# Performance work log

Hardware: AMD Instinct MI355X
Metric: run time of the kernel (lower is better)

## Reference

```python
import jax, jax.numpy as jnp
import numpy as np

B, T, D, H = 8, 2048, 1024, 128

def setup_inputs() -> dict:
    key = jax.random.key(0)
    ks = jax.random.split(key, 8)
    s = 1.0 / np.sqrt(D)
    return {
        "x": jax.random.normal(ks[0], (B, T, D), dtype=jnp.float32),
        "att": jax.random.normal(ks[1], (B, T, D), dtype=jnp.float32),
        "Wk": jax.random.uniform(ks[2], (D, H), minval=-s, maxval=s, dtype=jnp.float32),
        "bk": jax.random.uniform(ks[3], (H,), minval=-s, maxval=s, dtype=jnp.float32),
        "Wq": jax.random.uniform(ks[4], (D, H), minval=-s, maxval=s, dtype=jnp.float32),
        "bq": jax.random.uniform(ks[5], (H,), minval=-s, maxval=s, dtype=jnp.float32),
        "Wv": jax.random.uniform(ks[6], (D, H), minval=-s, maxval=s, dtype=jnp.float32),
        "bv": jax.random.uniform(ks[7], (H,), minval=-s, maxval=s, dtype=jnp.float32),
    }

def reference(x, att, Wk, bk, Wq, bq, Wv, bv):
    # k, q from `att`; v from `x` (as in the original module)
    k = jnp.einsum('btd,dh->bth', att, Wk) + bk   # [B,T,H]
    q = jnp.einsum('btd,dh->bth', att, Wq) + bq   # [B,T,H]
    v = jnp.einsum('btd,dh->bth', x, Wv) + bv     # [B,T,H]
    # Faithful to source: scores / head_size**(-0.5) == scores * sqrt(head_size)
    scale = jnp.asarray(k.shape[-1], jnp.float32) ** 0.5
    scores = jnp.einsum('bqh,bkh->bqk', q, k) * scale  # [B,T,T]
    att_mat = jax.nn.softmax(scores, axis=-1)
    # dropout p=0.0 -> identity (eval semantics)
    return jnp.einsum('bqk,bkh->bqh', att_mat, v)      # [B,T,H]
```

## Files before the change

kernel.cpp:

```cpp
#include <hip/hip_runtime.h>
#include <stdint.h>

typedef unsigned short u16;
typedef __attribute__((ext_vector_type(8))) short bf16x8;
typedef __attribute__((ext_vector_type(4))) float f32x4;
typedef __attribute__((ext_vector_type(16))) float f32x16;
typedef __attribute__((ext_vector_type(4))) uint32_t u32x4;
typedef __attribute__((ext_vector_type(2))) int int2v;

#define T_LEN 2048
#define D_DIM 1024
#define H_DIM 128
#define SCALE_LOG2 16.32223116f

#define EXP2F(x) __builtin_amdgcn_exp2f(x)

__device__ __forceinline__ u16 f2bf(float f) {
  uint32_t u = __float_as_uint(f);
  u += 0x7FFFu + ((u >> 16) & 1u);
  return (u16)(u >> 16);
}
__device__ __forceinline__ float bf2f(u16 h) { return __uint_as_float(((uint32_t)h) << 16); }

__device__ __forceinline__ void gload16(const void* g, void* l) {
  __builtin_amdgcn_global_load_lds(
      (const __attribute__((address_space(1))) uint32_t*)(uintptr_t)g,
      (__attribute__((address_space(3))) uint32_t*)(uint32_t)(uintptr_t)l,
      16, 0, 0);
}

#define VMCNT0() asm volatile("s_waitcnt vmcnt(0)" ::: "memory")
#define VMLG0() asm volatile("s_waitcnt vmcnt(0) lgkmcnt(0)" ::: "memory")
#define BAR() __builtin_amdgcn_s_barrier()
#define PRIO(n) __builtin_amdgcn_s_setprio(n)

#define MFMA(a, b, c) __builtin_amdgcn_mfma_f32_16x16x32_bf16((a), (b), (c), 0, 0, 0)
#define MFMA32(a, b, c) __builtin_amdgcn_mfma_f32_32x32x16_bf16((a), (b), (c), 0, 0, 0)

__device__ __forceinline__ uint32_t cvtpk(float lo, float hi) {
  uint32_t r;
  asm("v_cvt_pk_bf16_f32 %0, %1, %2" : "=v"(r) : "v"(lo), "v"(hi));
  return r;
}
__device__ __forceinline__ void plswap(uint32_t& a, uint32_t& b, int hi) {
#if __has_builtin(__builtin_amdgcn_permlane32_swap)
  int2v r = __builtin_amdgcn_permlane32_swap((int)a, (int)b, false, false);
  a = (uint32_t)r.x;
  b = (uint32_t)r.y;
#else
  uint32_t as = (uint32_t)__shfl_xor((int)a, 32);
  uint32_t bs = (uint32_t)__shfl_xor((int)b, 32);
  uint32_t na = hi ? bs : a;
  uint32_t nb = hi ? b : as;
  a = na;
  b = nb;
#endif
}

__global__ __launch_bounds__(256) void prep_w(
    const float* __restrict__ Wk, const float* __restrict__ Wq, const float* __restrict__ Wv,
    u16* __restrict__ wqh, u16* __restrict__ wql,
    u16* __restrict__ wkh, u16* __restrict__ wkl,
    u16* __restrict__ wvh) {
  __shared__ u16 th[3][128][16];
  __shared__ u16 tl[2][128][16];
  const int i = threadIdx.x;
  const int d0 = blockIdx.x * 16;
  const int dl = i >> 4;
  const int hb = (i & 15) * 8;
  const int d = d0 + dl;
#pragma unroll
  for (int e = 0; e < 8; ++e) {
    int h = hb + e;
    float q = Wq[d * H_DIM + h] * SCALE_LOG2;
    float k = Wk[d * H_DIM + h];
    float v = Wv[d * H_DIM + h];
    u16 qh = f2bf(q); th[0][h][dl] = qh; tl[0][h][dl] = f2bf(q - bf2f(qh));
    u16 kh = f2bf(k); th[1][h][dl] = kh; tl[1][h][dl] = f2bf(k - bf2f(kh));
    th[2][h][dl] = f2bf(v);
  }
  __syncthreads();
  const int h = i >> 1, c = i & 1;
  u16* planes[5] = {wqh, wql, wkh, wkl, wvh};
  const u16* srcs[5] = {&th[0][0][0], &tl[0][0][0], &th[1][0][0], &tl[1][0][0], &th[2][0][0]};
#pragma unroll
  for (int p = 0; p < 5; ++p) {
    bf16x8 v8 = *(const bf16x8*)(srcs[p] + h * 16 + c * 8);
    *(bf16x8*)(planes[p] + h * 1024 + d0 + c * 8) = v8;
  }
}

#define QBUF 53248

__global__ __launch_bounds__(512) void qkv_proj(
    const float* __restrict__ att, const float* __restrict__ x,
    const u16* __restrict__ wqh, const u16* __restrict__ wql,
    const u16* __restrict__ wkh, const u16* __restrict__ wkl,
    const u16* __restrict__ wvh,
    const float* __restrict__ bq, const float* __restrict__ bk, const float* __restrict__ bv,
    u16* __restrict__ qhp, u16* __restrict__ qlp,
    u16* __restrict__ khp, u16* __restrict__ klp,
    u16* __restrict__ vtp) {
  __shared__ __attribute__((aligned(128))) char lds[104 * 1024];

  const int tid = threadIdx.x;
  const int wid = tid >> 6;
  const int ln = tid & 63;
  const int g = ln >> 4;
  const int cl = ln & 15;
  const int t0g = blockIdx.x * 64;

  const f32x4 fz = {0.f, 0.f, 0.f, 0.f};
  f32x4 accq[4], acck[4], accv[4];
#pragma unroll
  for (int s = 0; s < 4; ++s) { accq[s] = fz; acck[s] = fz; accv[s] = fz; }

  const int isA = tid < 256;
  const int at = tid & 255;
  const int arow = at >> 2;
  const int ac = at & 3;
  const float* srcp = (isA ? att : x) + (size_t)(t0g + arow) * D_DIM + ac * 8;
  const int aw_off = (isA ? 0 : 8192) + arow * 64 + ((ac ^ ((arow >> 1) & 3)) * 16);

  auto STAGE_W = [&](int b, int ks) {
    char* wt = lds + b * QBUF + 12288;
#pragma unroll
    for (int j = 0; j < 5; ++j) {
      int seg = wid * 5 + j;
      int p = seg >> 3;
      int s = seg & 7;
      int db = s * 1024 + ln * 16;
      int row = db >> 6;
      int c = (db >> 4) & 3;
      int cs = c ^ ((row >> 1) & 3);
      const u16* wp = (p == 0) ? wqh : (p == 1) ? wql : (p == 2) ? wkh : (p == 3) ? wkl : wvh;
      gload16(wp + row * 1024 + ks * 32 + cs * 8, wt + p * 8192 + s * 1024);
    }
  };
  auto CWRITE_A = [&](int b, f32x4 f0, f32x4 f1) {
    bf16x8 vh, vl;
#pragma unroll
    for (int e = 0; e < 4; ++e) {
      u16 h0 = f2bf(f0[e]); vh[e] = (short)h0; vl[e] = (short)f2bf(f0[e] - bf2f(h0));
      u16 h1 = f2bf(f1[e]); vh[e + 4] = (short)h1; vl[e + 4] = (short)f2bf(f1[e] - bf2f(h1));
    }
    char* dst = lds + b * QBUF + aw_off;
    *(bf16x8*)dst = vh;
    if (isA) *(bf16x8*)(dst + 4096) = vl;
  };

  {
    f32x4 f0 = *(const f32x4*)(srcp);
    f32x4 f1 = *(const f32x4*)(srcp + 4);
    STAGE_W(0, 0);
    CWRITE_A(0, f0, f1);
  }
  f32x4 pA0 = *(const f32x4*)(srcp + 32);
  f32x4 pA1 = *(const f32x4*)(srcp + 36);
  VMLG0();
  BAR();

  int cur = 0;
  for (int ks = 0; ks < 32; ++ks) {
    f32x4 nA0, nA1;
    if (ks < 30) {
      nA0 = *(const f32x4*)(srcp + (ks + 2) * 32);
      nA1 = *(const f32x4*)(srcp + (ks + 2) * 32 + 4);
    }
    if (ks < 31) STAGE_W(cur ^ 1, ks + 1);
    char* base = lds + cur * QBUF;
    char* wt = base + 12288;
    bf16x8 ah[4], al[4], xh[4];
#pragma unroll
    for (int s = 0; s < 4; ++s) {
      int row = s * 16 + cl;
      int byte = row * 64 + ((g ^ ((row >> 1) & 3)) * 16);
      ah[s] = *(const bf16x8*)(base + byte);
      al[s] = *(const bf16x8*)(base + 4096 + byte);
      xh[s] = *(const bf16x8*)(base + 8192 + byte);
    }
    {
      int hrow = wid * 16 + cl;
      int wb = hrow * 64 + ((g ^ ((hrow >> 1) & 3)) * 16);
      bf16x8 bqh_ = *(const bf16x8*)(wt + 0 * 8192 + wb);
      bf16x8 bql_ = *(const bf16x8*)(wt + 1 * 8192 + wb);
      bf16x8 bkh_ = *(const bf16x8*)(wt + 2 * 8192 + wb);
      bf16x8 bkl_ = *(const bf16x8*)(wt + 3 * 8192 + wb);
      bf16x8 bvh_ = *(const bf16x8*)(wt + 4 * 8192 + wb);
      PRIO(1);
#pragma unroll
      for (int s = 0; s < 4; ++s) {
        accq[s] = MFMA(ah[s], bqh_, accq[s]);
        accq[s] = MFMA(al[s], bqh_, accq[s]);
        accq[s] = MFMA(ah[s], bql_, accq[s]);
        acck[s] = MFMA(ah[s], bkh_, acck[s]);
        acck[s] = MFMA(al[s], bkh_, acck[s]);
        acck[s] = MFMA(ah[s], bkl_, acck[s]);
        accv[s] = MFMA(xh[s], bvh_, accv[s]);
      }
      PRIO(0);
    }
    if (ks < 31) CWRITE_A(cur ^ 1, pA0, pA1);
    pA0 = nA0;
    pA1 = nA1;
    VMLG0();
    BAR();
    cur ^= 1;
  }

  char* vbuf = lds;
  {
    int h = wid * 16 + cl;
    float bqv = bq[h] * SCALE_LOG2, bkv = bk[h], bvv = bv[h];
#pragma unroll
    for (int s = 0; s < 4; ++s) {
#pragma unroll
      for (int r = 0; r < 4; ++r) {
        int t = s * 16 + g * 4 + r;
        size_t idx = (size_t)(t0g + t) * H_DIM + h;
        float qv = accq[s][r] + bqv;
        u16 qh_ = f2bf(qv);
        qhp[idx] = qh_;
        qlp[idx] = f2bf(qv - bf2f(qh_));
        float kv = acck[s][r] + bkv;
        u16 kh_ = f2bf(kv);
        khp[idx] = kh_;
        klp[idx] = f2bf(kv - bf2f(kh_));
        float vv = accv[s][r] + bvv;
        int c3 = t >> 3;
        int byte = h * 128 + ((c3 ^ (h & 7)) * 16) + (t & 7) * 2;
        *(u16*)(vbuf + byte) = f2bf(vv);
      }
    }
  }
  __syncthreads();
  {
    int h = tid >> 2, qtr = tid & 3;
    int b2 = t0g >> 11;
    int tb = t0g & 2047;
    u16* dst = vtp + ((size_t)(b2 * H_DIM + h)) * T_LEN + tb + qtr * 16;
#pragma unroll
    for (int c2 = 0; c2 < 2; ++c2) {
      int c3 = qtr * 2 + c2;
      bf16x8 v8 = *(const bf16x8*)(vbuf + h * 128 + ((c3 ^ (h & 7)) * 16));
      *(bf16x8*)(dst + c2 * 8) = v8;
    }
  }
}

#define KVB 32
#define NT 16

__global__ __launch_bounds__(512, 2) void attn(
    const u16* __restrict__ qhp, const u16* __restrict__ qlp,
    const u16* __restrict__ khp, const u16* __restrict__ klp,
    const u16* __restrict__ vtp,
    float* __restrict__ out) {
  __shared__ __attribute__((aligned(128))) char lds[128 * 1024];

  const int tid = threadIdx.x;
  const int w = tid >> 6;
  const int l = tid & 63;
  const int q5 = l & 31;
  const int hi = l >> 5;
  const int wq = w >> 2;
  const int kvq = w & 3;
  const int pi = wq;
  const int bid = blockIdx.x;
  const int b_ = bid & 7;
  const int t0 = (bid >> 3) * 64;
  const int qrow = t0 + wq * 32 + q5;
  const int kv0q = kvq * 512;

  bf16x8 qh[8], ql[8];
  {
    const u16* qb = qhp + (size_t)(b_ * T_LEN + qrow) * H_DIM + hi * 8;
    const u16* qlb = qlp + (size_t)(b_ * T_LEN + qrow) * H_DIM + hi * 8;
#pragma unroll
    for (int kc = 0; kc < 8; ++kc) {
      qh[kc] = *(const bf16x8*)(qb + kc * 16);
      ql[kc] = *(const bf16x8*)(qlb + kc * 16);
    }
  }

  uint32_t sgoff[8];
#pragma unroll
  for (int i = 0; i < 8; ++i) {
    int gid = i * 128 + pi * 64 + l;
    int plane = gid >> 9;
    int n = gid & 511;
    int row = n >> 4;
    int slot = n & 15;
    int dg = slot ^ (row & 15);
    sgoff[i] = (uint32_t)(plane * 2097152 + (b_ * T_LEN + row) * H_DIM + dg * 8);
  }
  char* const qbuf0 = lds + kvq * 2 * 16384;

  auto STAGE = [&](int b, int kvoff) {
    char* buf = qbuf0 + b * 16384;
#pragma unroll
    for (int i = 0; i < 8; ++i)
      gload16(khp + sgoff[i] + (uint32_t)(kvoff * H_DIM), buf + i * 2048 + pi * 1024);
  };

  f32x16 o[4] = {};
  float m_ = -1e30f;
  float l_ = 0.f;

  STAGE(0, kv0q);
  VMCNT0();
  BAR();

  int cur = 0;
  for (int t = 0; t < NT; ++t) {
    if (t < NT - 1) STAGE(cur ^ 1, kv0q + (t + 1) * KVB);
    bf16x8 vfr[8];
#pragma unroll
    for (int ks = 0; ks < 2; ++ks)
#pragma unroll
      for (int nt = 0; nt < 4; ++nt)
        vfr[ks * 4 + nt] = *(const bf16x8*)(
            vtp + (size_t)(b_ * H_DIM + nt * 32 + q5) * T_LEN +
            kv0q + t * KVB + ks * 16 + hi * 8);

    const char* kb = qbuf0 + cur * 16384 + q5 * 256;
    f32x16 s0 = {}, s1 = {}, s2 = {};
    PRIO(1);
#pragma unroll
    for (int kc = 0; kc < 8; ++kc) {
      int slot = (((kc * 2 + hi) ^ (q5 & 15)) * 16);
      bf16x8 kh_f = *(const bf16x8*)(kb + slot);
      bf16x8 kl_f = *(const bf16x8*)(kb + 8192 + slot);
      s0 = MFMA32(kh_f, qh[kc], s0);
      s1 = MFMA32(kl_f, qh[kc], s1);
      s2 = MFMA32(kh_f, ql[kc], s2);
    }
    PRIO(0);
    f32x16 s = (s0 + s1) + s2;

    float pmax = s[0];
#pragma unroll
    for (int j = 1; j < 16; ++j) pmax = fmaxf(pmax, s[j]);
    pmax = fmaxf(pmax, __shfl_xor(pmax, 32));
    if (__any(pmax > m_ + 8.f)) {
      float mn = fmaxf(m_, pmax);
      float sf = EXP2F(m_ - mn);
      m_ = mn;
      l_ *= sf;
#pragma unroll
      for (int j = 0; j < 16; ++j) {
        int rj = (j & 3) + 8 * (j >> 2) + 4 * hi;
        float sfj = __shfl(sf, rj);
        o[0][j] *= sfj; o[1][j] *= sfj; o[2][j] *= sfj; o[3][j] *= sfj;
      }
    }
    float p[16];
#pragma unroll
    for (int j = 0; j < 16; ++j) p[j] = EXP2F(s[j] - m_);
    float ps = 0.f;
#pragma unroll
    for (int j = 0; j < 16; ++j) ps += p[j];
    ps += __shfl_xor(ps, 32);
    l_ += ps;

    uint32_t u0 = cvtpk(p[0], p[1]), v0 = cvtpk(p[4], p[5]);
    uint32_t u1 = cvtpk(p[2], p[3]), v1 = cvtpk(p[6], p[7]);
    uint32_t u2 = cvtpk(p[8], p[9]), v2 = cvtpk(p[12], p[13]);
    uint32_t u3 = cvtpk(p[10], p[11]), v3 = cvtpk(p[14], p[15]);
    plswap(u0, v0, hi);
    plswap(u1, v1, hi);
    plswap(u2, v2, hi);
    plswap(u3, v3, hi);
    u32x4 f0w = {u0, u1, v0, v1};
    u32x4 f1w = {u2, u3, v2, v3};
    bf16x8 pa0 = *(bf16x8*)&f0w;
    bf16x8 pa1 = *(bf16x8*)&f1w;

    PRIO(1);
#pragma unroll
    for (int nt = 0; nt < 4; ++nt) o[nt] = MFMA32(pa0, vfr[nt], o[nt]);
#pragma unroll
    for (int nt = 0; nt < 4; ++nt) o[nt] = MFMA32(pa1, vfr[4 + nt], o[nt]);
    PRIO(0);

    VMCNT0();
    BAR();
    cur ^= 1;
  }

  float* mlb = (float*)(lds + 96 * 1024);
  __syncthreads();
  if (hi == 0) {
    mlb[(wq * 4 + kvq) * 64 + q5 * 2] = m_;
    mlb[(wq * 4 + kvq) * 64 + q5 * 2 + 1] = l_;
  }
  __syncthreads();
  float sc;
  {
    float ms0 = mlb[(wq * 4 + 0) * 64 + q5 * 2], ls0 = mlb[(wq * 4 + 0) * 64 + q5 * 2 + 1];
    float ms1 = mlb[(wq * 4 + 1) * 64 + q5 * 2], ls1 = mlb[(wq * 4 + 1) * 64 + q5 * 2 + 1];
    float ms2 = mlb[(wq * 4 + 2) * 64 + q5 * 2], ls2 = mlb[(wq * 4 + 2) * 64 + q5 * 2 + 1];
    float ms3 = mlb[(wq * 4 + 3) * 64 + q5 * 2], ls3 = mlb[(wq * 4 + 3) * 64 + q5 * 2 + 1];
    float mM = fmaxf(fmaxf(ms0, ms1), fmaxf(ms2, ms3));
    float L = ls0 * EXP2F(ms0 - mM) + ls1 * EXP2F(ms1 - mM) +
              ls2 * EXP2F(ms2 - mM) + ls3 * EXP2F(ms3 - mM);
    sc = EXP2F(m_ - mM) / L;
  }
#pragma unroll
  for (int j = 0; j < 16; ++j) {
    int rj = (j & 3) + 8 * (j >> 2) + 4 * hi;
    float scj = __shfl(sc, rj);
    o[0][j] *= scj; o[1][j] *= scj; o[2][j] *= scj; o[3][j] *= scj;
  }
  if (kvq != 0) {
    float* ob = (float*)(lds + (wq * 3 + (kvq - 1)) * 16384);
#pragma unroll
    for (int nt = 0; nt < 4; ++nt)
#pragma unroll
      for (int j = 0; j < 16; ++j) ob[nt * 1024 + j * 64 + l] = o[nt][j];
  }
  __syncthreads();
  if (kvq == 0) {
    float* ob0 = (float*)(lds + (wq * 3 + 0) * 16384);
    float* ob1 = (float*)(lds + (wq * 3 + 1) * 16384);
    float* ob2 = (float*)(lds + (wq * 3 + 2) * 16384);
#pragma unroll
    for (int j = 0; j < 16; ++j) {
      int rj = (j & 3) + 8 * (j >> 2) + 4 * hi;
      size_t rbase = (size_t)(b_ * T_LEN + t0 + wq * 32 + rj) * H_DIM + q5;
#pragma unroll
      for (int nt = 0; nt < 4; ++nt) {
        int oi = nt * 1024 + j * 64 + l;
        out[rbase + nt * 32] = o[nt][j] + ob0[oi] + ob1[oi] + ob2[oi];
      }
    }
  }
}

extern "C" void kernel_launch(void* const* d_in, const int* in_sizes, int n_in,
                              void* d_out, int out_size, void* d_ws, size_t ws_size,
                              hipStream_t stream) {
  const float* x   = (const float*)d_in[0];
  const float* att = (const float*)d_in[1];
  const float* Wk  = (const float*)d_in[2];
  const float* bk  = (const float*)d_in[3];
  const float* Wq  = (const float*)d_in[4];
  const float* bq  = (const float*)d_in[5];
  const float* Wv  = (const float*)d_in[6];
  const float* bv  = (const float*)d_in[7];
  float* out = (float*)d_out;
  char* ws = (char*)d_ws;

  u16* wqh = (u16*)(ws);
  u16* wql = (u16*)(ws + 256 * 1024);
  u16* wkh = (u16*)(ws + 512 * 1024);
  u16* wkl = (u16*)(ws + 768 * 1024);
  u16* wvh = (u16*)(ws + 1024 * 1024);
  u16* qhp = (u16*)(ws + (size_t)2 * 1024 * 1024);
  u16* qlp = (u16*)(ws + (size_t)6 * 1024 * 1024);
  u16* khp = (u16*)(ws + (size_t)10 * 1024 * 1024);
  u16* klp = (u16*)(ws + (size_t)14 * 1024 * 1024);
  u16* vtp = (u16*)(ws + (size_t)18 * 1024 * 1024);

  prep_w<<<64, 256, 0, stream>>>(Wk, Wq, Wv, wqh, wql, wkh, wkl, wvh);
  qkv_proj<<<256, 512, 0, stream>>>(att, x, wqh, wql, wkh, wkl, wvh,
                                    bq, bk, bv, qhp, qlp, khp, klp, vtp);
  attn<<<256, 512, 0, stream>>>(qhp, qlp, khp, klp, vtp, out);
}
```

Baseline: 264.0 us.

## Software-pipeline attention so QK of next tile overlaps softmax/PV of previous

The attention loop is restructured so each iteration computes the QK^T scores for tile t while running the softmax and PV MFMAs for tile t-1. V fragments for the previous tile are loaded late, and the trailing tile is drained after the loop. The explicit vmcnt(0) wait per iteration is dropped and relies on the in-order vmcnt implied by the V-fragment use. Separately, the projection loop issues its weight staging earlier and waits only to vmcnt(2) so the prefetched activation loads stay in flight. The max and sum reductions are also rewritten as trees. The pipelining raises register pressure, since a score tile and V fragments are live together, and it depends on the load-ordering assumptions for correctness.

```diff
diff --git a/kernel.cpp b/kernel.cpp
--- a/kernel.cpp
+++ b/kernel.cpp
@@ -31,6 +31,7 @@
 
 #define VMCNT0() asm volatile("s_waitcnt vmcnt(0)" ::: "memory")
 #define VMLG0() asm volatile("s_waitcnt vmcnt(0) lgkmcnt(0)" ::: "memory")
+#define VM2LG0() asm volatile("s_waitcnt vmcnt(2) lgkmcnt(0)" ::: "memory")
 #define BAR() __builtin_amdgcn_s_barrier()
 #define PRIO(n) __builtin_amdgcn_s_setprio(n)
 
@@ -162,12 +163,12 @@
 
   int cur = 0;
   for (int ks = 0; ks < 32; ++ks) {
+    if (ks < 31) STAGE_W(cur ^ 1, ks + 1);
     f32x4 nA0, nA1;
     if (ks < 30) {
       nA0 = *(const f32x4*)(srcp + (ks + 2) * 32);
       nA1 = *(const f32x4*)(srcp + (ks + 2) * 32 + 4);
     }
-    if (ks < 31) STAGE_W(cur ^ 1, ks + 1);
     char* base = lds + cur * QBUF;
     char* wt = base + 12288;
     bf16x8 ah[4], al[4], xh[4];
@@ -203,7 +204,7 @@
     if (ks < 31) CWRITE_A(cur ^ 1, pA0, pA1);
     pA0 = nA0;
     pA1 = nA1;
-    VMLG0();
+    if (ks < 30) VM2LG0(); else VMLG0();
     BAR();
     cur ^= 1;
   }
@@ -306,41 +307,16 @@
   f32x16 o[4] = {};
   float m_ = -1e30f;
   float l_ = 0.f;
-
-  STAGE(0, kv0q);
-  VMCNT0();
-  BAR();
-
-  int cur = 0;
-  for (int t = 0; t < NT; ++t) {
-    if (t < NT - 1) STAGE(cur ^ 1, kv0q + (t + 1) * KVB);
-    bf16x8 vfr[8];
-#pragma unroll
-    for (int ks = 0; ks < 2; ++ks)
-#pragma unroll
-      for (int nt = 0; nt < 4; ++nt)
-        vfr[ks * 4 + nt] = *(const bf16x8*)(
-            vtp + (size_t)(b_ * H_DIM + nt * 32 + q5) * T_LEN +
-            kv0q + t * KVB + ks * 16 + hi * 8);
-
-    const char* kb = qbuf0 + cur * 16384 + q5 * 256;
-    f32x16 s0 = {}, s1 = {}, s2 = {};
-    PRIO(1);
-#pragma unroll
-    for (int kc = 0; kc < 8; ++kc) {
-      int slot = (((kc * 2 + hi) ^ (q5 & 15)) * 16);
-      bf16x8 kh_f = *(const bf16x8*)(kb + slot);
-      bf16x8 kl_f = *(const bf16x8*)(kb + 8192 + slot);
-      s0 = MFMA32(kh_f, qh[kc], s0);
-      s1 = MFMA32(kl_f, qh[kc], s1);
-      s2 = MFMA32(kh_f, ql[kc], s2);
-    }
-    PRIO(0);
-    f32x16 s = (s0 + s1) + s2;
-
-    float pmax = s[0];
-#pragma unroll
-    for (int j = 1; j < 16; ++j) pmax = fmaxf(pmax, s[j]);
+  f32x16 s_prev;
+
+  auto SMPV = [&](const bf16x8* vfr) {
+    float t01 = fmaxf(s_prev[0], s_prev[1]), t23 = fmaxf(s_prev[2], s_prev[3]);
+    float t45 = fmaxf(s_prev[4], s_prev[5]), t67 = fmaxf(s_prev[6], s_prev[7]);
+    float t89 = fmaxf(s_prev[8], s_prev[9]), tab = fmaxf(s_prev[10], s_prev[11]);
+    float tcd = fmaxf(s_prev[12], s_prev[13]), tef = fmaxf(s_prev[14], s_prev[15]);
+    float q0 = fmaxf(t01, t23), q1 = fmaxf(t45, t67);
+    float q2 = fmaxf(t89, tab), q3 = fmaxf(tcd, tef);
+    float pmax = fmaxf(fmaxf(q0, q1), fmaxf(q2, q3));
     pmax = fmaxf(pmax, __shfl_xor(pmax, 32));
     if (__any(pmax > m_ + 8.f)) {
       float mn = fmaxf(m_, pmax);
@@ -356,10 +332,11 @@
     }
     float p[16];
 #pragma unroll
-    for (int j = 0; j < 16; ++j) p[j] = EXP2F(s[j] - m_);
-    float ps = 0.f;
-#pragma unroll
-    for (int j = 0; j < 16; ++j) ps += p[j];
+    for (int j = 0; j < 16; ++j) p[j] = EXP2F(s_prev[j] - m_);
+    float a0 = p[0] + p[1], a1 = p[2] + p[3], a2 = p[4] + p[5], a3 = p[6] + p[7];
+    float a4 = p[8] + p[9], a5 = p[10] + p[11], a6 = p[12] + p[13], a7 = p[14] + p[15];
+    float b0 = a0 + a1, b1 = a2 + a3, b2 = a4 + a5, b3 = a6 + a7;
+    float ps = (b0 + b1) + (b2 + b3);
     ps += __shfl_xor(ps, 32);
     l_ += ps;
 
@@ -375,17 +352,56 @@
     u32x4 f1w = {u2, u3, v2, v3};
     bf16x8 pa0 = *(bf16x8*)&f0w;
     bf16x8 pa1 = *(bf16x8*)&f1w;
-
+#pragma unroll
+    for (int nt = 0; nt < 4; ++nt) o[nt] = MFMA32(pa0, vfr[nt], o[nt]);
+#pragma unroll
+    for (int nt = 0; nt < 4; ++nt) o[nt] = MFMA32(pa1, vfr[4 + nt], o[nt]);
+  };
+
+  auto LOADV = [&](int tv, bf16x8* vfr) {
+#pragma unroll
+    for (int ks = 0; ks < 2; ++ks)
+#pragma unroll
+      for (int nt = 0; nt < 4; ++nt)
+        vfr[ks * 4 + nt] = *(const bf16x8*)(
+            vtp + (size_t)(b_ * H_DIM + nt * 32 + q5) * T_LEN +
+            kv0q + tv * KVB + ks * 16 + hi * 8);
+  };
+
+  STAGE(0, kv0q);
+  VMCNT0();
+  BAR();
+
+  for (int t = 0; t < NT; ++t) {
+    if (t + 1 < NT) STAGE((t + 1) & 1, kv0q + (t + 1) * KVB);
+    bf16x8 vfr[8];
+    if (t > 0) LOADV(t - 1, vfr);
+
+    const char* kb = qbuf0 + (t & 1) * 16384 + q5 * 256;
+    f32x16 s0 = {}, s1 = {}, s2 = {};
     PRIO(1);
 #pragma unroll
-    for (int nt = 0; nt < 4; ++nt) o[nt] = MFMA32(pa0, vfr[nt], o[nt]);
-#pragma unroll
-    for (int nt = 0; nt < 4; ++nt) o[nt] = MFMA32(pa1, vfr[4 + nt], o[nt]);
+    for (int kc = 0; kc < 8; ++kc) {
+      int slot = (((kc * 2 + hi) ^ (q5 & 15)) * 16);
+      bf16x8 kh_f = *(const bf16x8*)(kb + slot);
+      bf16x8 kl_f = *(const bf16x8*)(kb + 8192 + slot);
+      s0 = MFMA32(kh_f, qh[kc], s0);
+      s1 = MFMA32(kl_f, qh[kc], s1);
+      s2 = MFMA32(kh_f, ql[kc], s2);
+    }
     PRIO(0);
 
-    VMCNT0();
+    if (t > 0) SMPV(vfr);
+
+    s_prev = (s0 + s1) + s2;
+    if (t == 0) VMCNT0();
     BAR();
-    cur ^= 1;
+  }
+
+  {
+    bf16x8 vfr[8];
+    LOADV(NT - 1, vfr);
+    SMPV(vfr);
   }
 
   float* mlb = (float*)(lds + 96 * 1024);
```

Measured after the change: 274.9 us. 4.1% more time.
